# Performance work log

Measured on AMD Instinct MI355X. Metric: run time of the kernel, lower is better.

## Reference

```python
import jax, jax.numpy as jnp
import numpy as np

B, S, V, E, H, L = 32, 64, 96, 256, 512, 3
DIN = 2 * H  # padded input width for stacked LSTM weight tensors


def _cell(x, h, c, Wih, Whh, bih, bhh):
    # PyTorch LSTMCell gate order: i, f, g, o
    g = x @ Wih.T + h @ Whh.T + bih + bhh
    i, f, gg, o = jnp.split(g, 4, axis=-1)
    c2 = jax.nn.sigmoid(f) * c + jax.nn.sigmoid(i) * jnp.tanh(gg)
    h2 = jax.nn.sigmoid(o) * jnp.tanh(c2)
    return h2, c2


def _pad_feat(x, d):
    p = d - x.shape[-1]
    return x if p == 0 else jnp.pad(x, ((0, 0),) * (x.ndim - 1) + ((0, p),))


def _run_lstm(xs, Wih, Whh, bih, bhh, reverse):
    # xs: [S, B, Din]
    if reverse:
        xs = xs[::-1]
    b = xs.shape[1]
    init = (jnp.zeros((b, H), xs.dtype), jnp.zeros((b, H), xs.dtype))

    def step(carry, xt):
        h, c = _cell(xt, carry[0], carry[1], Wih, Whh, bih, bhh)
        return (h, c), h

    (h, c), ys = jax.lax.scan(step, init, xs)
    if reverse:
        ys = ys[::-1]
    return ys, h, c


def setup_inputs():
    key = jax.random.key(0)
    ks = jax.random.split(key, 20)
    f = lambda k, shp, s=0.08: jax.random.normal(k, shp, jnp.float32) * s
    return {
        "src": jax.random.randint(ks[0], (B, S), 0, V - 1),  # avoids padding_idx=95
        "trg": jax.random.randint(ks[1], (B, S), 0, V - 1),
        "embedding": f(ks[2], (V, E), 0.5),
        "enc_Wih": f(ks[3], (L, 2, 4 * H, DIN)),
        "enc_Whh": f(ks[4], (L, 2, 4 * H, H)),
        "enc_bih": f(ks[5], (L, 2, 4 * H)),
        "enc_bhh": f(ks[6], (L, 2, 4 * H)),
        "dec_Wih": f(ks[7], (L, 4 * H, DIN)),
        "dec_Whh": f(ks[8], (L, 4 * H, H)),
        "dec_bih": f(ks[9], (L, 4 * H)),
        "dec_bhh": f(ks[10], (L, 4 * H)),
        "attn_W": f(ks[11], (H, 3 * H)),
        "attn_b": f(ks[12], (H,)),
        "attn_v": jax.random.uniform(ks[13], (H,), jnp.float32),
        "proj_W": f(ks[14], (2 * H, E + 2 * H)),
        "proj_b": f(ks[15], (2 * H,)),
        "fc_W": f(ks[16], (V, H)),
        "fc_b": f(ks[17], (V,)),
    }


def _forward(src, trg, embedding, enc_Wih, enc_Whh, enc_bih, enc_bhh,
             dec_Wih, dec_Whh, dec_bih, dec_bhh, attn_W, attn_b, attn_v,
             proj_W, proj_b, fc_W, fc_b):
    emb = embedding[src]                 # [B,S,E]; dropout=identity (eval)
    xs = emb.transpose(1, 0, 2)          # [S,B,E]
    h_sum, c_sum = [], []
    for l in range(L):
        xin = _pad_feat(xs, DIN)         # zero-pad so stacked weights apply; padded cols hit zeros
        yf, hf, cf = _run_lstm(xin, enc_Wih[l, 0], enc_Whh[l, 0], enc_bih[l, 0], enc_bhh[l, 0], False)
        yb, hb, cb = _run_lstm(xin, enc_Wih[l, 1], enc_Whh[l, 1], enc_bih[l, 1], enc_bhh[l, 1], True)
        xs = jnp.concatenate([yf, yb], -1)  # [S,B,2H]
        h_sum.append(hf + hb)
        c_sum.append(cf + cb)            # hidden.view(L,2,B,H).sum(dim=1)
    enc_out = xs.transpose(1, 0, 2)      # [B,S,2H]
    dec_h, dec_c = jnp.stack(h_sum), jnp.stack(c_sum)  # [L,B,H]

    tokens = trg[:, :-1].T               # teacher_forcing_ratio = 1.0 (deterministic)

    def dec_step(carry, tok):
        h, c = carry
        htop = h[-1]                     # [B,H]
        rep = jnp.concatenate([jnp.broadcast_to(htop[:, None, :], (B, S, H)), enc_out], -1)
        energy = jnp.tanh(rep @ attn_W.T + attn_b)               # [B,S,H]
        attn = jax.nn.softmax(jnp.einsum('d,bsd->bs', attn_v, energy), axis=1)
        context = jnp.einsum('bs,bsd->bd', attn, enc_out)        # [B,2H]
        x = jnp.concatenate([embedding[tok], context], -1) @ proj_W.T + proj_b  # [B,2H]
        hs, cs = [], []
        xin = x
        for l in range(L):
            hl, cl = _cell(_pad_feat(xin, DIN), h[l], c[l], dec_Wih[l], dec_Whh[l], dec_bih[l], dec_bhh[l])
            hs.append(hl)
            cs.append(cl)
            xin = hl
        out = xin @ fc_W.T + fc_b        # [B,V]
        return (jnp.stack(hs), jnp.stack(cs)), out

    _, outs = jax.lax.scan(dec_step, (dec_h, dec_c), tokens)     # [S-1,B,V]
    outputs = jnp.concatenate([jnp.zeros((1, B, V), outs.dtype), outs], 0)
    return outputs.transpose(1, 0, 2)    # [B,S,V]; t=0 row is zeros, matching torch


def reference(src, trg, embedding, enc_Wih, enc_Whh, enc_bih, enc_bhh,
              dec_Wih, dec_Whh, dec_bih, dec_bhh, attn_W, attn_b, attn_v,
              proj_W, proj_b, fc_W, fc_b):
    return _forward(src, trg, embedding, enc_Wih, enc_Whh, enc_bih, enc_bhh,
                    dec_Wih, dec_Whh, dec_bih, dec_bhh, attn_W, attn_b, attn_v,
                    proj_W, proj_b, fc_W, fc_b)
```

## Files before the change

### kernel.cpp

```cpp
#include <hip/hip_runtime.h>

#define B_ 32
#define S_ 64
#define V_ 96
#define E_ 256
#define H_ 512
#define L_ 3
#define DIN_ 1024
#define G4_ 2048
#define BH_ (B_*H_)
#define BDIN_ (B_*DIN_)
#define FSTRIDE 16

typedef unsigned short u16;

__device__ __forceinline__ float bfu(u16 u){ return __uint_as_float(((unsigned)u) << 16); }
__device__ __forceinline__ u16 f2b(float f){
  unsigned x = __float_as_uint(f);
  unsigned r = (x + 0x7FFFu + ((x >> 16) & 1u)) >> 16;
  return (u16)r;
}
__device__ __forceinline__ float sigm(float x){ return 1.f/(1.f+__expf(-x)); }
__device__ __forceinline__ float bsum(float a){
  #pragma unroll
// ... 101 lines not shown
    Bs[bkk+2][bnn]=wv.z; Bs[bkk+3][bnn]=wv.w;
    __syncthreads();
    #pragma unroll
    for(int kk=0;kk<16;kk++){
      const float4 av0 = *(const float4*)&As[kk][ty*8];
      const float4 av1 = *(const float4*)&As[kk][ty*8+4];
      const float4 bv  = *(const float4*)&Bs[kk][tx*4];
      float am[8] = {av0.x,av0.y,av0.z,av0.w,av1.x,av1.y,av1.z,av1.w};
      float bn[4] = {bv.x,bv.y,bv.z,bv.w};
      #pragma unroll
      for(int i=0;i<8;i++){
        #pragma unroll
        for(int j=0;j<4;j++) acc[i][j] = fmaf(am[i], bn[j], acc[i][j]);
      }
    }
    __syncthreads();
  }
  float bias[4];
  #pragma unroll
  for(int j=0;j<4;j++){
    float bb = 0.f;
    if(b1) bb += LD<BF>(b1, o1 + n0 + tx*4 + j);
    if(b2) bb += LD<BF>(b2, o2 + n0 + tx*4 + j);
    bias[j] = bb;
  }
  #pragma unroll
  for(int i=0;i<8;i++){
    float* cp = C + (size_t)(m0 + ty*8 + i)*ldc + (n0 + tx*4);
    #pragma unroll
    for(int j=0;j<4;j++) cp[j] = acc[i][j] + bias[j];
  }
}
__global__ __launch_bounds__(256) void k_gemm(
  const float* A, int lda, const void* W, int ldw, size_t woff,
  const void* b1, size_t o1, const void* b2, size_t o2,
  float* C, int ldc, int K, const int* fl)
{
  if(*fl) gemm_body<1>(A,lda,W,ldw,woff,b1,o1,b2,o2,C,ldc,K);
  else    gemm_body<0>(A,lda,W,ldw,woff,b1,o1,b2,o2,C,ldc,K);
}

__global__ void k_outzero(void* __restrict__ out, const int* fl){
  int i = blockIdx.x*256 + threadIdx.x;
  if(i < B_*V_){
    int b = i / V_, v = i % V_;
    size_t idx = (size_t)b*(S_*V_) + v;
    if(*fl) ((u16*)out)[idx] = 0;
    else    ((float*)out)[idx] = 0.f;
  }
}

struct EncArgs2 {
  const float* G;
  const void* Whh; size_t oWh;
  float* henc;
  float* cT;
  float* Xout;
  float* dh0;
  float* dcT;
  int l;
  const int* fl;
  int* flags; int gbase;
};

template<int BF>
__device__ void enc2_body(const EncArgs2& a){
  __shared__ float SM[16384];
  const int tid  = threadIdx.x;
  const int lane = tid & 63;
  const int wid  = tid >> 6;
  const int w4   = (blockIdx.x<<2) + (wid & 3);
  const int j    = w4 & 511;
  const int d    = w4 >> 9;
  const int half = wid >> 2;
  int g = a.gbase;

  float wh[4][8];
  #pragma unroll
  for(int gg=0; gg<4; gg++){
    size_t rowh = a.oWh + ((size_t)d*G4_ + (size_t)gg*H_ + j)*H_;
    #pragma unroll
    for(int p=0;p<2;p++){
      float4 v = LD4<BF>(a.Whh, rowh + (lane<<2) + p*256);
      wh[gg][p*4+0]=v.x; wh[gg][p*4+1]=v.y; wh[gg][p*4+2]=v.z; wh[gg][p*4+3]=v.w;
    }
  }
  const bool own = (lane < 32) && ((lane>>4) == half);
  const size_t ci = ((size_t)d*H_ + j)*32 + (lane & 31);
  float cv = 0.f;

  for(int p=0;p<64;p++){
    const int t = d ? (63-p) : p;
    if(p == 0){
      for(int i=tid<<2; i<BH_; i+=2048) *(float4*)&SM[i] = make_float4(0.f,0.f,0.f,0.f);
    } else {
      const float* hsrc = a.henc + (size_t)((p&63)*2 + d)*BH_;
      for(int i=tid<<2; i<BH_; i+=2048) *(float4*)&SM[i] = *(const float4*)&hsrc[i];
    }
    __syncthreads();

    const int bE = lane & 31;
    const float* Gp = a.G + (size_t)(t*B_+bE)*4096 + (size_t)d*G4_ + j;
    float pg0=Gp[0], pg1=Gp[512], pg2=Gp[1024], pg3=Gp[1536];

    float gv0=0.f, gv1=0.f, gv2=0.f, gv3=0.f;
    for(int b=half*16; b<half*16+16; b++){
      float gs[4] = {0.f,0.f,0.f,0.f};
      const float* hp = &SM[(b<<9) + (lane<<2)];
      #pragma unroll
      for(int pp=0;pp<2;pp++){
        float4 hv = *(const float4*)(hp + pp*256);
        float ha[4] = {hv.x,hv.y,hv.z,hv.w};
        #pragma unroll
        for(int gg=0;gg<4;gg++){
          #pragma unroll
          for(int i=0;i<4;i++) gs[gg] = fmaf(ha[i], wh[gg][pp*4+i], gs[gg]);
        }
      }
      #pragma unroll
      for(int gg=0;gg<4;gg++) gs[gg] = bsum(gs[gg]);
      if(lane == b){ gv0=gs[0]; gv1=gs[1]; gv2=gs[2]; gv3=gs[3]; }
    }
    if(own){
      float gi = gv0+pg0, gf = gv1+pg1, gG = gv2+pg2, go = gv3+pg3;
      float c2 = sigm(gf)*cv + sigm(gi)*tanhf(gG);
      float h2 = sigm(go)*tanhf(c2);
      cv = c2;
      stc(&a.henc[(size_t)(((p+1)&63)*2 + d)*BH_ + (size_t)lane*H_ + j], h2);
      a.Xout[(size_t)(t*B_+lane)*DIN_ + (d<<9) + j] = h2;
    }
    gbar(a.flags, ++g);
  }
  if(own) stc(&a.cT[ci], cv);
  gbar(a.flags, ++g);
  for(int i = blockIdx.x*512 + tid; i < BH_; i += 131072){
    float hf2 = a.henc[(size_t)(0*2+0)*BH_ + i];
    float hb2 = a.henc[(size_t)(0*2+1)*BH_ + i];
    a.dh0[(size_t)a.l*BH_ + i] = hf2 + hb2;
    a.dcT[(size_t)a.l*BH_ + i] = ldc(&a.cT[i]) + ldc(&a.cT[BH_ + i]);
  }
}
__global__ __launch_bounds__(512,1) void k_enc2(EncArgs2 a){
  if(*a.fl) enc2_body<1>(a); else enc2_body<0>(a);
}

struct DecArgs2 {
  const int* trg;
  const void* emb; const void* aW; const void* av; const void* pW; const void* pb;
  const void* dWih; const void* dWhh; const void* dbih; const void* dbhh;
  const void* fW; const void* fb;
  const float* Epre; const float* X3;
  const float* dh0;
  float* dhb;
  float* zb;
  u16*   ctxb;
  float* xpb;
  const float* dcT;
  void* out;
  const int* fl;
  int* flags; int gbase;
};

template<int BF, int CP>
__device__ __forceinline__ void dec_loadW(const DecArgs2& a, const int l,
    const int jp, const int lane, const int half,
    float wx[2][16], float wh[2][8], float pg[2]){
  #pragma unroll
  for(int gg=0; gg<2; gg++){
    const int gr = half*2 + gg;
    size_t rowx = ((size_t)l*G4_ + (size_t)gr*H_ + jp)*DIN_;
    #pragma unroll
    for(int p=0;p<CP;p++){
      float4 v = LD4<BF>(a.dWih, rowx + (lane<<2) + p*256);
      wx[gg][p*4+0]=v.x; wx[gg][p*4+1]=v.y; wx[gg][p*4+2]=v.z; wx[gg][p*4+3]=v.w;
    }
    size_t rowh = ((size_t)l*G4_ + (size_t)gr*H_ + jp)*H_;
    #pragma unroll
    for(int p=0;p<2;p++){
      float4 v = LD4<BF>(a.dWhh, rowh + (lane<<2) + p*256);
      wh[gg][p*4+0]=v.x; wh[gg][p*4+1]=v.y; wh[gg][p*4+2]=v.z; wh[gg][p*4+3]=v.w;
    }
    size_t bb = (size_t)l*G4_ + (size_t)gr*H_ + jp;
    pg[gg] = LD<BF>(a.dbih, bb) + LD<BF>(a.dbhh, bb);
  }
}

template<int BF, int CP>
__device__ __forceinline__ void dec_cellG(const DecArgs2& a, float* SM,
    const int t, const int l, const int jp, const int bh, const int bh_blk,
    const int lane, const int tid, const int half, const int pairid,
    float wx[2][16], float wh[2][8], float pg[2], float& cv){
  constexpr int Kx  = CP*256;
  constexpr int HB  = (CP==4) ? 2 : 1;
  constexpr int NBs = 16/HB;
  const float* xsrc = (l==0) ? (a.xpb + (size_t)t*BDIN_ + (size_t)bh_blk*16*DIN_)
                             : (a.dhb + (size_t)((t+1)*3 + (l-1))*BH_ + (size_t)bh_blk*16*H_);
  const float* hsrc = (t==0) ? (a.dh0 + (size_t)l*BH_ + (size_t)bh_blk*16*H_)
                             : (a.dhb + (size_t)(t*3 + l)*BH_ + (size_t)bh_blk*16*H_);
  float gvA=0.f, gvB=0.f;
  #pragma unroll
  for(int hf=0; hf<HB; hf++){
    const float* xg = xsrc + (size_t)hf*NBs*Kx;
    const float* hg = hsrc + (size_t)hf*NBs*H_;
    for(int i=tid<<2; i<NBs*Kx; i+=2048) *(float4*)&SM[i] = *(const float4*)&xg[i];
    for(int i=tid<<2; i<NBs*H_; i+=2048) *(float4*)&SM[NBs*Kx + i] = *(const float4*)&hg[i];
    __syncthreads();
    for(int ib2=0; ib2<NBs; ib2++){
      const int ib = hf*NBs + ib2;
      float g0a=0.f,g0b=0.f,g1a=0.f,g1b=0.f;
      const float* xr = &SM[ib2*Kx + (lane<<2)];
      #pragma unroll
      for(int p=0;p<CP;p++){
        float4 xv = *(const float4*)(xr + p*256);
        if(p & 1){
          g0b = fmaf(xv.x, wx[0][p*4+0], g0b); g0b = fmaf(xv.y, wx[0][p*4+1], g0b);
          g0b = fmaf(xv.z, wx[0][p*4+2], g0b); g0b = fmaf(xv.w, wx[0][p*4+3], g0b);
          g1b = fmaf(xv.x, wx[1][p*4+0], g1b); g1b = fmaf(xv.y, wx[1][p*4+1], g1b);
          g1b = fmaf(xv.z, wx[1][p*4+2], g1b); g1b = fmaf(xv.w, wx[1][p*4+3], g1b);
        } else {
          g0a = fmaf(xv.x, wx[0][p*4+0], g0a); g0a = fmaf(xv.y, wx[0][p*4+1], g0a);
          g0a = fmaf(xv.z, wx[0][p*4+2], g0a); g0a = fmaf(xv.w, wx[0][p*4+3], g0a);
          g1a = fmaf(xv.x, wx[1][p*4+0], g1a); g1a = fmaf(xv.y, wx[1][p*4+1], g1a);
          g1a = fmaf(xv.z, wx[1][p*4+2], g1a); g1a = fmaf(xv.w, wx[1][p*4+3], g1a);
        }
      }
      const float* hr = &SM[NBs*Kx + ib2*H_ + (lane<<2)];
      {
        float4 hv = *(const float4*)(hr);
        g0a = fmaf(hv.x, wh[0][0], g0a); g0a = fmaf(hv.y, wh[0][1], g0a);
        g0a = fmaf(hv.z, wh[0][2], g0a); g0a = fmaf(hv.w, wh[0][3], g0a);
        g1a = fmaf(hv.x, wh[1][0], g1a); g1a = fmaf(hv.y, wh[1][1], g1a);
        g1a = fmaf(hv.z, wh[1][2], g1a); g1a = fmaf(hv.w, wh[1][3], g1a);
      }
      {
        float4 hv = *(const float4*)(hr + 256);
        g0b = fmaf(hv.x, wh[0][4], g0b); g0b = fmaf(hv.y, wh[0][5], g0b);
        g0b = fmaf(hv.z, wh[0][6], g0b); g0b = fmaf(hv.w, wh[0][7], g0b);
        g1b = fmaf(hv.x, wh[1][4], g1b); g1b = fmaf(hv.y, wh[1][5], g1b);
        g1b = fmaf(hv.z, wh[1][6], g1b); g1b = fmaf(hv.w, wh[1][7], g1b);
      }
      float gs0 = bsum(g0a + g0b);
      float gs1 = bsum(g1a + g1b);
      if(lane == ib){ gvA=gs0; gvB=gs1; }
    }
    __syncthreads();
  }
  float* comb = SM + 15360 + pairid*128;
  if(lane < 16){
    comb[half*32 + lane*2 + 0] = gvA + pg[0];
    comb[half*32 + lane*2 + 1] = gvB + pg[1];
  }
  __syncthreads();
  if(half == 0 && lane < 16){
    const int b = bh*16 + lane;
    float gi = comb[lane*2 + 0];
    float gf = comb[lane*2 + 1];
    float gG = comb[32 + lane*2 + 0];
    float go = comb[32 + lane*2 + 1];
    float c2 = sigm(gf)*cv + sigm(gi)*tanhf(gG);
    float h2 = sigm(go)*tanhf(c2);
    cv = c2;
    stc(&a.dhb[(size_t)((t+1)*3 + l)*BH_ + (size_t)b*H_ + jp], h2);
  }
}

template<int BF>
__device__ void dec2_body(const DecArgs2& a){
  __shared__ float SM[16384];
  const int tid  = threadIdx.x;
  const int lane = tid & 63;
  const int wid  = tid >> 6;
  const int w4   = (blockIdx.x<<2) + (wid & 3);
  const int jp   = w4 & 511;
  const int bh   = w4 >> 9;
  const int half = wid >> 2;
  const int pairid = wid & 3;
  const int bh_blk = blockIdx.x >> 7;
  int g = a.gbase;

  float cvs[3];
  #pragma unroll
  for(int l=0;l<3;l++)
    cvs[l] = a.dcT[((size_t)l*H_ + jp)*32 + (size_t)bh*16 + (lane&15)];

  float wx[2][16], wh[2][8], pg[2];

  for(int t=0; t<64; ++t){
    {
      const float* hs = (t==0) ? (a.dh0 + (size_t)2*BH_ + (size_t)bh_blk*16*H_)
                               : (a.dhb + (size_t)(t*3 + 2)*BH_ + (size_t)bh_blk*16*H_);
      for(int i=tid<<2; i<16*H_; i+=2048) *(float4*)&SM[i] = *(const float4*)&hs[i];
      __syncthreads();
      if(t < 63){
        float wz[8];
        size_t rz = (size_t)jp*1536;
        #pragma unroll
        for(int p=0;p<2;p++){
          float4 v = LD4<BF>(a.aW, rz + (lane<<2) + p*256);
          wz[p*4+0]=v.x; wz[p*4+1]=v.y; wz[p*4+2]=v.z; wz[p*4+3]=v.w;
        }
        for(int ib=half*8; ib<half*8+8; ib++){
          const float* hp = &SM[(ib<<9) + (lane<<2)];
          float aa = 0.f, ab = 0.f;
          {
            float4 hv = *(const float4*)(hp);
            aa = fmaf(hv.x, wz[0], aa); aa = fmaf(hv.y, wz[1], aa);
            aa = fmaf(hv.z, wz[2], aa); aa = fmaf(hv.w, wz[3], aa);
          }
          {
            float4 hv = *(const float4*)(hp + 256);
            ab = fmaf(hv.x, wz[4], ab); ab = fmaf(hv.y, wz[5], ab);
            ab = fmaf(hv.z, wz[6], ab); ab = fmaf(hv.w, wz[7], ab);
          }
          float acc = bsum(aa + ab);
          if(lane==0) stc(&a.zb[(size_t)t*BH_ + (size_t)(bh*16+ib)*H_ + jp], acc);
        }
      }
      if(t > 0){
        #pragma unroll
        for(int r=0;r<3;r++){
          const int q  = jp + (r<<9);
          const int v_ = q % 96;
          const int ib = q / 96;
          if((ib>>3) != half) continue;
          float wf[8];
          size_t rf = (size_t)v_*H_;
          #pragma unroll
          for(int p=0;p<2;p++){
            float4 v = LD4<BF>(a.fW, rf + (lane<<2) + p*256);
            wf[p*4+0]=v.x; wf[p*4+1]=v.y; wf[p*4+2]=v.z; wf[p*4+3]=v.w;
          }
          const float* hp = &SM[(ib<<9) + (lane<<2)];
          float aa = 0.f, ab = 0.f;
          {
            float4 hv = *(const float4*)(hp);
            aa = fmaf(hv.x, wf[0], aa); aa = fmaf(hv.y, wf[1], aa);
            aa = fmaf(hv.z, wf[2], aa); aa = fmaf(hv.w, wf[3], aa);
          }
          {
            float4 hv = *(const float4*)(hp + 256);
            ab = fmaf(hv.x, wf[4], ab); ab = fmaf(hv.y, wf[5], ab);
            ab = fmaf(hv.z, wf[6], ab); ab = fmaf(hv.w, wf[7], ab);
          }
          float acc = bsum(aa + ab);
          if(lane==0){
            float rr = acc + LD<BF>(a.fb, v_);
            size_t oi = (size_t)(bh*16+ib)*(S_*V_) + (size_t)t*V_ + v_;
            if constexpr(BF) ((u16*)a.out)[oi] = f2b(rr);
            else             ((float*)a.out)[oi] = rr;
          }
        }
      }
    }
    if(t == 63) break;
    gbar(a.flags, ++g);

    {
      const int b  = blockIdx.x >> 3;
      const int ss = blockIdx.x & 7;
      float* Zs = SM; float* Ss = SM + 512;
      Zs[tid] = a.zb[(size_t)t*BH_ + (size_t)b*H_ + tid];
      __syncthreads();
      float wa[8];
      #pragma unroll
      for(int p=0;p<2;p++){
        float4 v = LD4<BF>(a.av, (lane<<2) + p*256);
        wa[p*4+0]=v.x; wa[p*4+1]=v.y; wa[p*4+2]=v.z; wa[p*4+3]=v.w;
      }
      for(int s=wid; s<64; s+=8){
        const float* ep = a.Epre + ((size_t)(s*B_ + b))*H_;
        float acc = 0.f;
        #pragma unroll
        for(int p=0;p<2;p++){
          const float4 e4 = *(const float4*)(ep + (lane<<2) + p*256);
          const float4 z4 = *(const float4*)(Zs + (lane<<2) + p*256);
          acc = fmaf(wa[p*4+0], tanhf(e4.x+z4.x), acc);
          acc = fmaf(wa[p*4+1], tanhf(e4.y+z4.y), acc);
          acc = fmaf(wa[p*4+2], tanhf(e4.z+z4.z), acc);
          acc = fmaf(wa[p*4+3], tanhf(e4.w+z4.w), acc);
        }
        acc = bsum(acc);
        if(lane==0) Ss[s] = acc;
      }
      __syncthreads();
      if(tid < 64){
        float vv = Ss[tid];
        float m = vv;
        #pragma unroll
        for(int off=1; off<64; off<<=1) m = fmaxf(m, __shfl_xor(m, off));
        float e = __expf(vv - m);
        float su = e;
        #pragma unroll
        for(int off=1; off<64; off<<=1) su += __shfl_xor(su, off);
        Ss[tid] = e / su;
      }
      __syncthreads();
      if(tid < 32){
        const int d4 = ss*128 + (tid<<2);
        float a0=0.f,a1=0.f,a2=0.f,a3=0.f;
        float b0=0.f,b1=0.f,b2=0.f,b3=0.f;
        const float* xb = a.X3 + (size_t)b*DIN_ + d4;
        for(int s=0;s<64;s+=2){
          const float pp = Ss[s];
          const float qq = Ss[s+1];
          const float4 xv = *(const float4*)(xb + (size_t)s*BDIN_);
          const float4 yv = *(const float4*)(xb + (size_t)(s+1)*BDIN_);
          a0 = fmaf(pp, xv.x, a0); a1 = fmaf(pp, xv.y, a1);
          a2 = fmaf(pp, xv.z, a2); a3 = fmaf(pp, xv.w, a3);
          b0 = fmaf(qq, yv.x, b0); b1 = fmaf(qq, yv.y, b1);
          b2 = fmaf(qq, yv.z, b2); b3 = fmaf(qq, yv.w, b3);
        }
        a0 += b0; a1 += b1; a2 += b2; a3 += b3;
        u16* cp = a.ctxb + (size_t)t*BDIN_ + (size_t)b*DIN_ + d4;
        unsigned lo = (unsigned)f2b(a0) | ((unsigned)f2b(a1)<<16);
        unsigned hi = (unsigned)f2b(a2) | ((unsigned)f2b(a3)<<16);
        stci((int*)cp, (int)lo);
        stci(((int*)cp)+1, (int)hi);
      }
    }
    gbar(a.flags, ++g);

    {
      const u16* cs = a.ctxb + (size_t)t*BDIN_ + (size_t)bh_blk*16*DIN_;
      for(int i=tid*4; i<16*DIN_; i+=2048){
        ushort4 v = *(const ushort4*)(cs + i);
        *(float4*)&SM[i] = make_float4(bfu(v.x), bfu(v.y), bfu(v.z), bfu(v.w));
      }
      __syncthreads();
      float wpe[2][4], wpc[2][16];
      #pragma unroll
      for(int jj=0;jj<2;jj++){
        size_t row = (size_t)(jp + (jj<<9))*1280;
        float4 v = LD4<BF>(a.pW, row + (lane<<2));
        wpe[jj][0]=v.x; wpe[jj][1]=v.y; wpe[jj][2]=v.z; wpe[jj][3]=v.w;
        #pragma unroll
        for(int p=0;p<4;p++){
          float4 c4 = LD4<BF>(a.pW, row + 256 + (lane<<2) + p*256);
          wpc[jj][p*4+0]=c4.x; wpc[jj][p*4+1]=c4.y; wpc[jj][p*4+2]=c4.z; wpc[jj][p*4+3]=c4.w;
        }
      }
      const float pb0 = LD<BF>(a.pb, jp);
      const float pb1 = LD<BF>(a.pb, jp+512);
      for(int ib=half*8; ib<half*8+8; ib++){
        const int b = bh*16 + ib;
        const int tok = a.trg[b*S_ + t];
        float4 ev = LD4<BF>(a.emb, (size_t)tok*E_ + (lane<<2));
        float s0a=0.f, s0b=0.f, s1a=0.f, s1b=0.f;
        s0a = fmaf(ev.x, wpe[0][0], s0a); s0a = fmaf(ev.y, wpe[0][1], s0a);
        s0a = fmaf(ev.z, wpe[0][2], s0a); s0a = fmaf(ev.w, wpe[0][3], s0a);
        s1a = fmaf(ev.x, wpe[1][0], s1a); s1a = fmaf(ev.y, wpe[1][1], s1a);
        s1a = fmaf(ev.z, wpe[1][2], s1a); s1a = fmaf(ev.w, wpe[1][3], s1a);
        const float* cp = &SM[(ib<<10) + (lane<<2)];
        #pragma unroll
        for(int p=0;p<4;p++){
          float4 c4 = *(const float4*)(cp + p*256);
          if(p & 1){
            s0b = fmaf(c4.x, wpc[0][p*4+0], s0b); s0b = fmaf(c4.y, wpc[0][p*4+1], s0b);
            s0b = fmaf(c4.z, wpc[0][p*4+2], s0b); s0b = fmaf(c4.w, wpc[0][p*4+3], s0b);
            s1b = fmaf(c4.x, wpc[1][p*4+0], s1b); s1b = fmaf(c4.y, wpc[1][p*4+1], s1b);
            s1b = fmaf(c4.z, wpc[1][p*4+2], s1b); s1b = fmaf(c4.w, wpc[1][p*4+3], s1b);
          } else {
            s0a = fmaf(c4.x, wpc[0][p*4+0], s0a); s0a = fmaf(c4.y, wpc[0][p*4+1], s0a);
            s0a = fmaf(c4.z, wpc[0][p*4+2], s0a); s0a = fmaf(c4.w, wpc[0][p*4+3], s0a);
            s1a = fmaf(c4.x, wpc[1][p*4+0], s1a); s1a = fmaf(c4.y, wpc[1][p*4+1], s1a);
            s1a = fmaf(c4.z, wpc[1][p*4+2], s1a); s1a = fmaf(c4.w, wpc[1][p*4+3], s1a);
          }
        }
        float s0 = bsum(s0a + s0b);
        float s1 = bsum(s1a + s1b);
        if(lane==0){
          stc(&a.xpb[(size_t)t*BDIN_ + (size_t)b*DIN_ + jp],       s0 + pb0);
          stc(&a.xpb[(size_t)t*BDIN_ + (size_t)b*DIN_ + jp + 512], s1 + pb1);
        }
      }
      __syncthreads();
    }
    dec_loadW<BF,4>(a, 0, jp, lane, half, wx, wh, pg);
    gbar(a.flags, ++g);
    dec_cellG<BF,4>(a, SM, t, 0, jp, bh, bh_blk, lane, tid, half, pairid, wx, wh, pg, cvs[0]);
    dec_loadW<BF,2>(a, 1, jp, lane, half, wx, wh, pg);
    gbar(a.flags, ++g);
    dec_cellG<BF,2>(a, SM, t, 1, jp, bh, bh_blk, lane, tid, half, pairid, wx, wh, pg, cvs[1]);
    dec_loadW<BF,2>(a, 2, jp, lane, half, wx, wh, pg);
    gbar(a.flags, ++g);
    dec_cellG<BF,2>(a, SM, t, 2, jp, bh, bh_blk, lane, tid, half, pairid, wx, wh, pg, cvs[2]);
    gbar(a.flags, ++g);
  }
}
__global__ __launch_bounds__(512,1) void k_dec2(DecArgs2 a){
  if(*a.fl) dec2_body<1>(a); else dec2_body<0>(a);
}

struct EncArgsO {
  const float* G;
  const float* Xin;
  const void* Wih; size_t oWi;
  const void* Whh; size_t oWh;
  const void* bih; size_t obi;
  const void* bhh; size_t obh;
  float* hst; float* cT; float* Xout; float* dh; float* dcT;
  int l; const int* fl; int* flags; int gbase;
};

template<int BF, int CP>
__device__ void encO_body(const EncArgsO& a){
  __shared__ float SM[16384];
  const int tid  = threadIdx.x;
  const int w    = (blockIdx.x<<2) + (tid>>6);
  const int lane = tid & 63;
  const int d    = w >> 9;
  const int j    = w & 511;
  int g = a.gbase;

  float wh[4][8];
  #pragma unroll
  for(int gg=0; gg<4; gg++){
    size_t rowh = a.oWh + ((size_t)d*G4_ + (size_t)gg*H_ + j)*H_;
    #pragma unroll
    for(int p=0;p<2;p++){
      float4 v = LD4<BF>(a.Whh, rowh + (lane<<2) + p*256);
      wh[gg][p*4+0]=v.x; wh[gg][p*4+1]=v.y; wh[gg][p*4+2]=v.z; wh[gg][p*4+3]=v.w;
    }
  }
  float wxf[4][CP?CP*4:1];
  float pbias[4];
  if constexpr(CP>0){
    #pragma unroll
    for(int gg=0; gg<4; gg++){
      size_t rowx = a.oWi + ((size_t)d*G4_ + (size_t)gg*H_ + j)*DIN_;
      #pragma unroll
      for(int p=0;p<CP;p++){
        float4 v = LD4<BF>(a.Wih, rowx + (lane<<2) + p*256);
        wxf[gg][p*4+0]=v.x; wxf[gg][p*4+1]=v.y; wxf[gg][p*4+2]=v.z; wxf[gg][p*4+3]=v.w;
      }
    }
    size_t bb = (size_t)d*G4_ + j;
    #pragma unroll
    for(int gg=0;gg<4;gg++)
      pbias[gg] = LD<BF>(a.bih, a.obi + bb + (size_t)gg*H_)
                + LD<BF>(a.bhh, a.obh + bb + (size_t)gg*H_);
  }
  const int bE = lane & 31;
  const size_t ci = ((size_t)d*H_ + j)*32 + bE;
  float cv = 0.f;
  int cur = 0;
  for(int p=0;p<64;p++){
    const int t = d ? (63-p) : p;
    if(p == 0){
      for(int i=tid<<2; i<BH_; i+=1024) *(float4*)&SM[i] = make_float4(0.f,0.f,0.f,0.f);
    } else {
      const float* hsrc = a.hst + (size_t)((cur<<1)+d)*BH_;
      #pragma unroll 4
      for(int i=tid; i<BH_; i+=256) SM[i] = ldc(hsrc + i);
    }
    __syncthreads();
    float pg[4];
    if constexpr(CP==0){
      const float* Gp = a.G + (size_t)(t*B_+bE)*4096 + (size_t)d*G4_ + j;
      pg[0]=Gp[0]; pg[1]=Gp[512]; pg[2]=Gp[1024]; pg[3]=Gp[1536];
    } else {
      pg[0]=pbias[0]; pg[1]=pbias[1]; pg[2]=pbias[2]; pg[3]=pbias[3];
    }
    const float* xrow = nullptr;
    if constexpr(CP>0) xrow = a.Xin + (size_t)t*B_*DIN_;
    float gv0=0.f, gv1=0.f, gv2=0.f, gv3=0.f;
    for(int b=0;b<32;b++){
      float gs[4] = {0.f,0.f,0.f,0.f};
      const float* hp = &SM[(b<<9) + (lane<<2)];
      #pragma unroll
      for(int pp=0;pp<2;pp++){
        float4 hv = *(const float4*)(hp + pp*256);
        float ha[4] = {hv.x,hv.y,hv.z,hv.w};
// ... 212 lines not shown
            if constexpr(BF) ((u16*)a.out)[oi] = f2b(rr);
            else             ((float*)a.out)[oi] = rr;
          }
        }
      }
    }
    if(t == 63) break;
    gbar(a.flags, ++g);
    if(blockIdx.x < 32){
      const int b = blockIdx.x;
      float* Zs = SM; float* Ss = SM + 512;
      for(int i=tid; i<512; i+=256) Zs[i] = ldc(a.z + (size_t)b*H_ + i);
      __syncthreads();
      float wa[8];
      #pragma unroll
      for(int p=0;p<2;p++){
        float4 v = LD4<BF>(a.av, (lane<<2) + p*256);
        wa[p*4+0]=v.x; wa[p*4+1]=v.y; wa[p*4+2]=v.z; wa[p*4+3]=v.w;
      }
      const int ww = tid>>6;
      for(int s=ww; s<64; s+=4){
        const float* ep = a.Epre + ((size_t)(s*B_ + b))*H_;
        float acc = 0.f;
        #pragma unroll
        for(int p=0;p<2;p++){
          const float4 e4 = *(const float4*)(ep + (lane<<2) + p*256);
          const float4 z4 = *(const float4*)(Zs + (lane<<2) + p*256);
          acc = fmaf(wa[p*4+0], tanhf(e4.x+z4.x), acc);
          acc = fmaf(wa[p*4+1], tanhf(e4.y+z4.y), acc);
          acc = fmaf(wa[p*4+2], tanhf(e4.z+z4.z), acc);
          acc = fmaf(wa[p*4+3], tanhf(e4.w+z4.w), acc);
        }
        acc = bsum(acc);
        if(lane==0) Ss[s] = acc;
      }
      __syncthreads();
      if(tid < 64){
        float vv = Ss[tid];
        float m = vv;
        #pragma unroll
        for(int off=1; off<64; off<<=1) m = fmaxf(m, __shfl_xor(m, off));
        float e = __expf(vv - m);
        float su = e;
        #pragma unroll
        for(int off=1; off<64; off<<=1) su += __shfl_xor(su, off);
        Ss[tid] = e / su;
      }
      __syncthreads();
      for(int d4 = tid<<2; d4 < DIN_; d4 += 1024){
        float a0=0.f,a1=0.f,a2=0.f,a3=0.f;
        const float* xb = a.X3 + (size_t)b*DIN_ + d4;
        for(int s=0;s<64;s++){
          const float pp = Ss[s];
          const float4 xv = *(const float4*)(xb + (size_t)s*BDIN_);
          a0 = fmaf(pp, xv.x, a0); a1 = fmaf(pp, xv.y, a1);
          a2 = fmaf(pp, xv.z, a2); a3 = fmaf(pp, xv.w, a3);
        }
        float* cp = &a.ctx[(size_t)b*DIN_ + d4];
        stc(cp+0, a0); stc(cp+1, a1); stc(cp+2, a2); stc(cp+3, a3);
      }
    }
    gbar(a.flags, ++g);
    {
      const float* cs = a.ctx + (size_t)bh_blk*16*DIN_;
      #pragma unroll 4
      for(int i=tid; i<16*DIN_; i+=256) SM[i] = ldc(cs + i);
      __syncthreads();
      float wpe[2][4], wpc[2][16];
      #pragma unroll
      for(int jj=0;jj<2;jj++){
        size_t row = (size_t)(jp + (jj<<9))*1280;
        float4 v = LD4<BF>(a.pW, row + (lane<<2));
        wpe[jj][0]=v.x; wpe[jj][1]=v.y; wpe[jj][2]=v.z; wpe[jj][3]=v.w;
        #pragma unroll
        for(int p=0;p<4;p++){
          float4 c4 = LD4<BF>(a.pW, row + 256 + (lane<<2) + p*256);
          wpc[jj][p*4+0]=c4.x; wpc[jj][p*4+1]=c4.y; wpc[jj][p*4+2]=c4.z; wpc[jj][p*4+3]=c4.w;
        }
      }
      const float pb0 = LD<BF>(a.pb, jp);
      const float pb1 = LD<BF>(a.pb, jp+512);
      for(int ib=0; ib<16; ib++){
        const int b = bh*16 + ib;
        const int tok = a.trg[b*S_ + t];
        float4 ev = LD4<BF>(a.emb, (size_t)tok*E_ + (lane<<2));
        float ea[4] = {ev.x, ev.y, ev.z, ev.w};
        float s0=0.f, s1=0.f;
        #pragma unroll
        for(int i=0;i<4;i++){ s0 = fmaf(ea[i], wpe[0][i], s0); s1 = fmaf(ea[i], wpe[1][i], s1); }
        const float* cp = &SM[(ib<<10) + (lane<<2)];
        #pragma unroll
        for(int p=0;p<4;p++){
          float4 c4 = *(const float4*)(cp + p*256);
          float ca[4] = {c4.x,c4.y,c4.z,c4.w};
          #pragma unroll
          for(int i=0;i<4;i++){ s0 = fmaf(ca[i], wpc[0][p*4+i], s0); s1 = fmaf(ca[i], wpc[1][p*4+i], s1); }
        }
        s0 = bsum(s0); s1 = bsum(s1);
        if(lane==0){
          stc(&a.xp[(size_t)b*DIN_ + jp],       s0 + pb0);
          stc(&a.xp[(size_t)b*DIN_ + jp + 512], s1 + pb1);
        }
      }
    }
    gbar(a.flags, ++g);
    decO_cell<BF,4>(a, SM, 0, cur, jp, bh, bh_blk, lane, tid, g, cvs[0]);
    decO_cell<BF,2>(a, SM, 1, cur, jp, bh, bh_blk, lane, tid, g, cvs[1]);
    decO_cell<BF,2>(a, SM, 2, cur, jp, bh, bh_blk, lane, tid, g, cvs[2]);
    cur ^= 1;
  }
}
__global__ __launch_bounds__(256,2) void k_dec_persO(DecArgsO a){
  if(*a.fl) decO_body<1>(a); else decO_body<0>(a);
}

extern "C" void kernel_launch(void* const* d_in, const int* in_sizes, int n_in,
                              void* d_out, int out_size, void* d_ws, size_t ws_size,
                              hipStream_t stream){
  const int* src  = (const int*)d_in[0];
  const int* trg  = (const int*)d_in[1];
  const void* emb = d_in[2];
  const void* eWih= d_in[3];
  const void* eWhh= d_in[4];
  const void* ebih= d_in[5];
  const void* ebhh= d_in[6];
  const void* dWih= d_in[7];
  const void* dWhh= d_in[8];
  const void* dbih= d_in[9];
  const void* dbhh= d_in[10];
  const void* aW  = d_in[11];
  const void* ab  = d_in[12];
  const void* av  = d_in[13];
  const void* pW  = d_in[14];
  const void* pb  = d_in[15];
  const void* fW  = d_in[16];
  const void* fb  = d_in[17];

  char* base = (char*)d_ws;
  size_t off = 0;
  auto take = [&](size_t bytes)->char*{
    char* p = base + off; off = (off + bytes + 255) & ~(size_t)255; return p;
  };

  const size_t szX  = (size_t)2048*1024*4;
  const size_t szG  = (size_t)2048*4096*4;
  const size_t szE  = (size_t)2048*512*4;
  int planA = ws_size >= (size_t)53*1024*1024;

  if(planA){
    float* X    = (float*)take(szX);
    float* Xh   = (float*)take(szX);
    float* G    = (float*)take(szG);
    float* dhb  = G;
    float* zb   = dhb + (size_t)64*3*BH_;
    float* xpb  = zb  + (size_t)63*BH_;
    u16*   ctxb = (u16*)(xpb + (size_t)63*BDIN_);
    float* Epre = (float*)take(szE);
    float* cTe  = (float*)take((size_t)2*BH_*4);
    float* dh0  = (float*)take((size_t)3*BH_*4);
    float* dcT  = (float*)take((size_t)3*BH_*4);
    int* fl     = (int*)take(256);
    int* flags  = (int*)take((256*FSTRIDE + 16)*4);

    k_detect<<<1, 256, 0, stream>>>(av, fl, flags);
    k_embed<<<8192, 256, 0, stream>>>(src, emb, X, fl);

    for(int l=0;l<L_;l++){
      int K = (l==0) ? E_ : DIN_;
      k_gemm<<<dim3(64,16), 256, 0, stream>>>(X, DIN_,
          eWih, DIN_, (size_t)l*2*G4_*DIN_,
          ebih, (size_t)l*2*G4_, ebhh, (size_t)l*2*G4_,
          G, 4096, K, fl);
      EncArgs2 ea;
      ea.G = G; ea.Whh = eWhh; ea.oWh = (size_t)l*2*G4_*H_;
      ea.henc = Xh; ea.cT = cTe; ea.Xout = X;
      ea.dh0 = dh0; ea.dcT = dcT; ea.l = l;
      ea.fl = fl; ea.flags = flags; ea.gbase = l*65;
      k_enc2<<<256, 512, 0, stream>>>(ea);
    }
    k_gemm<<<dim3(8,16), 256, 0, stream>>>(X, DIN_,
        aW, 3*H_, (size_t)H_, ab, 0, nullptr, 0, Epre, H_, DIN_, fl);
    k_outzero<<<12, 256, 0, stream>>>(d_out, fl);

    DecArgs2 da;
    da.trg = trg; da.emb = emb; da.aW = aW; da.av = av; da.pW = pW; da.pb = pb;
    da.dWih = dWih; da.dWhh = dWhh; da.dbih = dbih; da.dbhh = dbhh;
    da.fW = fW; da.fb = fb;
    da.Epre = Epre; da.X3 = X;
    da.dh0 = dh0; da.dhb = dhb; da.zb = zb; da.ctxb = ctxb; da.xpb = xpb;
    da.dcT = dcT; da.out = d_out; da.fl = fl; da.flags = flags; da.gbase = 3*65;
    k_dec2<<<256, 512, 0, stream>>>(da);
  } else {
    float* XA   = (float*)take(szX);
    float* XB   = (float*)take(szX);
    float* Epre = (float*)take(szE);
    float* hst  = (float*)take((size_t)4*BH_*4);
    float* cTe  = (float*)take((size_t)2*BH_*4);
    float* dh   = (float*)take((size_t)6*BH_*4);
    float* dcT  = (float*)take((size_t)3*BH_*4);
    float* zbuf = (float*)take((size_t)BH_*4);
    float* ctx  = (float*)take((size_t)2*BH_*4);
    float* xp   = (float*)take((size_t)2*BH_*4);
    int* fl     = (int*)take(256);
    int* flags  = (int*)take((256*FSTRIDE + 16)*4);

    k_detect<<<1, 256, 0, stream>>>(av, fl, flags);
    k_embed<<<8192, 256, 0, stream>>>(src, emb, XA, fl);

    float* Xin = XA; float* Xout = XB;
    for(int l=0;l<L_;l++){
      EncArgsO ea;
      ea.G = nullptr; ea.Xin = Xin;
      ea.Wih = eWih; ea.oWi = (size_t)l*2*G4_*DIN_;
      ea.Whh = eWhh; ea.oWh = (size_t)l*2*G4_*H_;
      ea.bih = ebih; ea.obi = (size_t)l*2*G4_;
      ea.bhh = ebhh; ea.obh = (size_t)l*2*G4_;
      ea.hst = hst; ea.cT = cTe; ea.Xout = Xout;
      ea.dh = dh; ea.dcT = dcT; ea.l = l;
      ea.fl = fl; ea.flags = flags; ea.gbase = l*65;
      if(l == 0) k_enc_persF0<<<256, 256, 0, stream>>>(ea);
      else       k_enc_persF12<<<256, 256, 0, stream>>>(ea);
      float* tmp = Xin; Xin = Xout; Xout = tmp;
    }
    k_gemm<<<dim3(8,16), 256, 0, stream>>>(Xin, DIN_,
        aW, 3*H_, (size_t)H_, ab, 0, nullptr, 0, Epre, H_, DIN_, fl);
    k_outzero<<<12, 256, 0, stream>>>(d_out, fl);

    DecArgsO da;
    da.trg = trg; da.emb = emb; da.aW = aW; da.av = av; da.pW = pW; da.pb = pb;
    da.dWih = dWih; da.dWhh = dWhh; da.dbih = dbih; da.dbhh = dbhh;
    da.fW = fW; da.fb = fb;
    da.Epre = Epre; da.X3 = Xin;
    da.dh = dh; da.dcT = dcT; da.z = zbuf; da.ctx = ctx; da.xp = xp;
    da.out = d_out; da.fl = fl; da.flags = flags; da.gbase = 3*65;
    k_dec_persO<<<256, 256, 0, stream>>>(da);
  }
}
```

Baseline: 9.570 ms.

## Fuse attention query projection into per-batch blocks and drop a grid barrier

Moves the decoder's attention-query projection (h @ attn_W slice) and the output fc projection into the same 32 per-batch blocks that compute attention scores, softmax and context. This removes the zb global scratch buffer and one grid-wide barrier per decoder step. The trade-off is that only 32 of 256 blocks do this work. Each block now streams the full attention weight slice serially across its waves, so per-step latency may grow while the other blocks sit idle.

```diff
diff --git a/kernel.cpp b/kernel.cpp
--- a/kernel.cpp
+++ b/kernel.cpp
@@ -277,7 +277,6 @@
   const float* Epre; const float* X3;
   const float* dh0;
   float* dhb;
-  float* zb;
   u16*   ctxb;
   float* xpb;
   const float* dcT;
@@ -411,138 +410,119 @@
   float wx[2][16], wh[2][8], pg[2];
 
   for(int t=0; t<64; ++t){
-    {
-      const float* hs = (t==0) ? (a.dh0 + (size_t)2*BH_ + (size_t)bh_blk*16*H_)
-                               : (a.dhb + (size_t)(t*3 + 2)*BH_ + (size_t)bh_blk*16*H_);
-      for(int i=tid<<2; i<16*H_; i+=2048) *(float4*)&SM[i] = *(const float4*)&hs[i];
+    if(blockIdx.x < 32){
+      const int b = blockIdx.x;
+      float* Ht = SM;
+      float* Zs = SM + 512;
+      float* Ss = SM + 1024;
+      const float* hs = (t==0) ? (a.dh0 + (size_t)2*BH_ + (size_t)b*H_)
+                               : (a.dhb + (size_t)(t*3 + 2)*BH_ + (size_t)b*H_);
+      Ht[tid] = hs[tid];
       __syncthreads();
-      if(t < 63){
-        float wz[8];
-        size_t rz = (size_t)jp*1536;
-        #pragma unroll
-        for(int p=0;p<2;p++){
-          float4 v = LD4<BF>(a.aW, rz + (lane<<2) + p*256);
-          wz[p*4+0]=v.x; wz[p*4+1]=v.y; wz[p*4+2]=v.z; wz[p*4+3]=v.w;
-        }
-        for(int ib=half*8; ib<half*8+8; ib++){
-          const float* hp = &SM[(ib<<9) + (lane<<2)];
-          float aa = 0.f, ab = 0.f;
+      if(t > 0){
+        for(int v_ = wid*12; v_ < wid*12+12 && v_ < 96; v_++){
+          size_t rf = (size_t)v_*H_;
+          float aa=0.f, ab=0.f;
           {
-            float4 hv = *(const float4*)(hp);
-            aa = fmaf(hv.x, wz[0], aa); aa = fmaf(hv.y, wz[1], aa);
-            aa = fmaf(hv.z, wz[2], aa); aa = fmaf(hv.w, wz[3], aa);
+            float4 wv = LD4<BF>(a.fW, rf + (lane<<2));
+            const float4 hv = *(const float4*)(Ht + (lane<<2));
+            aa = fmaf(hv.x,wv.x,aa); aa = fmaf(hv.y,wv.y,aa);
+            aa = fmaf(hv.z,wv.z,aa); aa = fmaf(hv.w,wv.w,aa);
           }
           {
-            float4 hv = *(const float4*)(hp + 256);
-            ab = fmaf(hv.x, wz[4], ab); ab = fmaf(hv.y, wz[5], ab);
-            ab = fmaf(hv.z, wz[6], ab); ab = fmaf(hv.w, wz[7], ab);
-          }
-          float acc = bsum(aa + ab);
-          if(lane==0) stc(&a.zb[(size_t)t*BH_ + (size_t)(bh*16+ib)*H_ + jp], acc);
-        }
-      }
-      if(t > 0){
-        #pragma unroll
-        for(int r=0;r<3;r++){
-          const int q  = jp + (r<<9);
-          const int v_ = q % 96;
-          const int ib = q / 96;
-          if((ib>>3) != half) continue;
-          float wf[8];
-          size_t rf = (size_t)v_*H_;
-          #pragma unroll
-          for(int p=0;p<2;p++){
-            float4 v = LD4<BF>(a.fW, rf + (lane<<2) + p*256);
-            wf[p*4+0]=v.x; wf[p*4+1]=v.y; wf[p*4+2]=v.z; wf[p*4+3]=v.w;
-          }
-          const float* hp = &SM[(ib<<9) + (lane<<2)];
-          float aa = 0.f, ab = 0.f;
-          {
-            float4 hv = *(const float4*)(hp);
-            aa = fmaf(hv.x, wf[0], aa); aa = fmaf(hv.y, wf[1], aa);
-            aa = fmaf(hv.z, wf[2], aa); aa = fmaf(hv.w, wf[3], aa);
-          }
-          {
-            float4 hv = *(const float4*)(hp + 256);
-            ab = fmaf(hv.x, wf[4], ab); ab = fmaf(hv.y, wf[5], ab);
-            ab = fmaf(hv.z, wf[6], ab); ab = fmaf(hv.w, wf[7], ab);
+            float4 wv = LD4<BF>(a.fW, rf + (lane<<2) + 256);
+            const float4 hv = *(const float4*)(Ht + (lane<<2) + 256);
+            ab = fmaf(hv.x,wv.x,ab); ab = fmaf(hv.y,wv.y,ab);
+            ab = fmaf(hv.z,wv.z,ab); ab = fmaf(hv.w,wv.w,ab);
           }
           float acc = bsum(aa + ab);
           if(lane==0){
             float rr = acc + LD<BF>(a.fb, v_);
-            size_t oi = (size_t)(bh*16+ib)*(S_*V_) + (size_t)t*V_ + v_;
+            size_t oi = (size_t)b*(S_*V_) + (size_t)t*V_ + v_;
             if constexpr(BF) ((u16*)a.out)[oi] = f2b(rr);
             else             ((float*)a.out)[oi] = rr;
           }
         }
       }
+      if(t < 63){
+        for(int j_ = wid*64; j_ < wid*64+64; j_++){
+          size_t rz = (size_t)j_*1536;
+          float aa=0.f, ab=0.f;
+          {
+            float4 wv = LD4<BF>(a.aW, rz + (lane<<2));
+            const float4 hv = *(const float4*)(Ht + (lane<<2));
+            aa = fmaf(hv.x,wv.x,aa); aa = fmaf(hv.y,wv.y,aa);
+            aa = fmaf(hv.z,wv.z,aa); aa = fmaf(hv.w,wv.w,aa);
+          }
+          {
+            float4 wv = LD4<BF>(a.aW, rz + (lane<<2) + 256);
+            const float4 hv = *(const float4*)(Ht + (lane<<2) + 256);
+            ab = fmaf(hv.x,wv.x,ab); ab = fmaf(hv.y,wv.y,ab);
+            ab = fmaf(hv.z,wv.z,ab); ab = fmaf(hv.w,wv.w,ab);
+          }
+          float acc = bsum(aa + ab);
+          if(lane==0) Zs[j_] = acc;
+        }
+        __syncthreads();
+        float wa[8];
+        #pragma unroll
+        for(int p=0;p<2;p++){
+          float4 v = LD4<BF>(a.av, (lane<<2) + p*256);
+          wa[p*4+0]=v.x; wa[p*4+1]=v.y; wa[p*4+2]=v.z; wa[p*4+3]=v.w;
+        }
+        for(int s=wid*8; s<wid*8+8; s++){
+          const float* ep = a.Epre + ((size_t)(s*B_ + b))*H_;
+          float acc = 0.f;
+          #pragma unroll
+          for(int p=0;p<2;p++){
+            const float4 e4 = *(const float4*)(ep + (lane<<2) + p*256);
+            const float4 z4 = *(const float4*)(Zs + (lane<<2) + p*256);
+            acc = fmaf(wa[p*4+0], tanhf(e4.x+z4.x), acc);
+            acc = fmaf(wa[p*4+1], tanhf(e4.y+z4.y), acc);
+            acc = fmaf(wa[p*4+2], tanhf(e4.z+z4.z), acc);
+            acc = fmaf(wa[p*4+3], tanhf(e4.w+z4.w), acc);
+          }
+          acc = bsum(acc);
+          if(lane==0) Ss[s] = acc;
+        }
+        __syncthreads();
+        if(tid < 64){
+          float vv = Ss[tid];
+          float m = vv;
+          #pragma unroll
+          for(int off=1; off<64; off<<=1) m = fmaxf(m, __shfl_xor(m, off));
+          float e = __expf(vv - m);
+          float su = e;
+          #pragma unroll
+          for(int off=1; off<64; off<<=1) su += __shfl_xor(su, off);
+          Ss[tid] = e / su;
+        }
+        __syncthreads();
+        if(tid < 256){
+          const int d4 = tid<<2;
+          float a0=0.f,a1=0.f,a2=0.f,a3=0.f;
+          float b0=0.f,b1=0.f,b2=0.f,b3=0.f;
+          const float* xb = a.X3 + (size_t)b*DIN_ + d4;
+          for(int s=0;s<64;s+=2){
+            const float pp = Ss[s];
+            const float qq = Ss[s+1];
+            const float4 xv = *(const float4*)(xb + (size_t)s*BDIN_);
+            const float4 yv = *(const float4*)(xb + (size_t)(s+1)*BDIN_);
+            a0 = fmaf(pp, xv.x, a0); a1 = fmaf(pp, xv.y, a1);
+            a2 = fmaf(pp, xv.z, a2); a3 = fmaf(pp, xv.w, a3);
+            b0 = fmaf(qq, yv.x, b0); b1 = fmaf(qq, yv.y, b1);
+            b2 = fmaf(qq, yv.z, b2); b3 = fmaf(qq, yv.w, b3);
+          }
+          a0 += b0; a1 += b1; a2 += b2; a3 += b3;
+          u16* cp = a.ctxb + (size_t)t*BDIN_ + (size_t)b*DIN_ + d4;
+          unsigned lo = (unsigned)f2b(a0) | ((unsigned)f2b(a1)<<16);
+          unsigned hi = (unsigned)f2b(a2) | ((unsigned)f2b(a3)<<16);
+          stci((int*)cp, (int)lo);
+          stci(((int*)cp)+1, (int)hi);
+        }
+      }
     }
     if(t == 63) break;
-    gbar(a.flags, ++g);
-
-    {
-      const int b  = blockIdx.x >> 3;
-      const int ss = blockIdx.x & 7;
-      float* Zs = SM; float* Ss = SM + 512;
-      Zs[tid] = a.zb[(size_t)t*BH_ + (size_t)b*H_ + tid];
-      __syncthreads();
-      float wa[8];
-      #pragma unroll
-      for(int p=0;p<2;p++){
-        float4 v = LD4<BF>(a.av, (lane<<2) + p*256);
-        wa[p*4+0]=v.x; wa[p*4+1]=v.y; wa[p*4+2]=v.z; wa[p*4+3]=v.w;
-      }
-      for(int s=wid; s<64; s+=8){
-        const float* ep = a.Epre + ((size_t)(s*B_ + b))*H_;
-        float acc = 0.f;
-        #pragma unroll
-        for(int p=0;p<2;p++){
-          const float4 e4 = *(const float4*)(ep + (lane<<2) + p*256);
-          const float4 z4 = *(const float4*)(Zs + (lane<<2) + p*256);
-          acc = fmaf(wa[p*4+0], tanhf(e4.x+z4.x), acc);
-          acc = fmaf(wa[p*4+1], tanhf(e4.y+z4.y), acc);
-          acc = fmaf(wa[p*4+2], tanhf(e4.z+z4.z), acc);
-          acc = fmaf(wa[p*4+3], tanhf(e4.w+z4.w), acc);
-        }
-        acc = bsum(acc);
-        if(lane==0) Ss[s] = acc;
-      }
-      __syncthreads();
-      if(tid < 64){
-        float vv = Ss[tid];
-        float m = vv;
-        #pragma unroll
-        for(int off=1; off<64; off<<=1) m = fmaxf(m, __shfl_xor(m, off));
-        float e = __expf(vv - m);
-        float su = e;
-        #pragma unroll
-        for(int off=1; off<64; off<<=1) su += __shfl_xor(su, off);
-        Ss[tid] = e / su;
-      }
-      __syncthreads();
-      if(tid < 32){
-        const int d4 = ss*128 + (tid<<2);
-        float a0=0.f,a1=0.f,a2=0.f,a3=0.f;
-        float b0=0.f,b1=0.f,b2=0.f,b3=0.f;
-        const float* xb = a.X3 + (size_t)b*DIN_ + d4;
-        for(int s=0;s<64;s+=2){
-          const float pp = Ss[s];
-          const float qq = Ss[s+1];
-          const float4 xv = *(const float4*)(xb + (size_t)s*BDIN_);
-          const float4 yv = *(const float4*)(xb + (size_t)(s+1)*BDIN_);
-          a0 = fmaf(pp, xv.x, a0); a1 = fmaf(pp, xv.y, a1);
-          a2 = fmaf(pp, xv.z, a2); a3 = fmaf(pp, xv.w, a3);
-          b0 = fmaf(qq, yv.x, b0); b1 = fmaf(qq, yv.y, b1);
-          b2 = fmaf(qq, yv.z, b2); b3 = fmaf(qq, yv.w, b3);
-        }
-        a0 += b0; a1 += b1; a2 += b2; a3 += b3;
-        u16* cp = a.ctxb + (size_t)t*BDIN_ + (size_t)b*DIN_ + d4;
-        unsigned lo = (unsigned)f2b(a0) | ((unsigned)f2b(a1)<<16);
-        unsigned hi = (unsigned)f2b(a2) | ((unsigned)f2b(a3)<<16);
-        stci((int*)cp, (int)lo);
-        stci(((int*)cp)+1, (int)hi);
-      }
-    }
     gbar(a.flags, ++g);
 
     {
@@ -1061,8 +1041,7 @@
     float* Xh   = (float*)take(szX);
     float* G    = (float*)take(szG);
     float* dhb  = G;
-    float* zb   = dhb + (size_t)64*3*BH_;
-    float* xpb  = zb  + (size_t)63*BH_;
+    float* xpb  = dhb + (size_t)64*3*BH_;
     u16*   ctxb = (u16*)(xpb + (size_t)63*BDIN_);
     float* Epre = (float*)take(szE);
     float* cTe  = (float*)take((size_t)2*BH_*4);
@@ -1096,7 +1075,7 @@
     da.dWih = dWih; da.dWhh = dWhh; da.dbih = dbih; da.dbhh = dbhh;
     da.fW = fW; da.fb = fb;
     da.Epre = Epre; da.X3 = X;
-    da.dh0 = dh0; da.dhb = dhb; da.zb = zb; da.ctxb = ctxb; da.xpb = xpb;
+    da.dh0 = dh0; da.dhb = dhb; da.ctxb = ctxb; da.xpb = xpb;
     da.dcT = dcT; da.out = d_out; da.fl = fl; da.flags = flags; da.gbase = 3*65;
     k_dec2<<<256, 512, 0, stream>>>(da);
   } else {
```

Result: slower. 12.81 ms (+33.9%).
